# Kernel tuning notes

Measured on AMD Instinct MI355X. Metric: run time of the kernel, lower is better.

## Reference

```python
import jax, jax.numpy as jnp
import numpy as np

EPS = 1e-12
HEADS = 16
DIM_KEYS = 16
DIM_VALUES = 64


def l2norm(t):
    # matches F.normalize(t, p=2, dim=-1) with eps=1e-12
    n = jnp.linalg.norm(t, axis=-1, keepdims=True)
    return t / jnp.maximum(n, EPS)


def tanh_norm(t):
    n = jnp.linalg.norm(t, axis=-1, keepdims=True)
    return jnp.tanh(n) * (t / jnp.maximum(n, EPS))


def split_heads(x, h):
    # [b, n, h*d] -> [b, h, n, d]
    b, n, hd = x.shape
    return x.reshape(b, n, h, hd // h).transpose(0, 2, 1, 3)


def setup_inputs() -> dict:
    key = jax.random.key(0)
    k1, k2, k3, k4 = jax.random.split(key, 4)
    b, n, dim = 4, 2048, 1024
    dim_inner = (DIM_KEYS + DIM_VALUES) * HEADS  # 1280
    tokens = jax.random.normal(k1, (b, n, dim), dtype=jnp.float32)
    Wqg = jax.random.normal(k2, (dim, dim_inner), dtype=jnp.float32) * (dim ** -0.5)
    Wkv = jax.random.normal(k3, (dim, dim_inner), dtype=jnp.float32) * (dim ** -0.5)
    Wout = jax.random.normal(k4, (DIM_VALUES * HEADS, dim), dtype=jnp.float32) * ((DIM_VALUES * HEADS) ** -0.5)
    return {"tokens": tokens, "Wqg": Wqg, "Wkv": Wkv, "Wout": Wout}


def reference(tokens, Wqg, Wkv, Wout):
    # self-attention variant: context = tokens, mask = None
    qg = split_heads(tokens @ Wqg, HEADS)   # [b, h, n, dk+dv]
    kv = split_heads(tokens @ Wkv, HEADS)
    queries, gates = qg[..., :DIM_KEYS], qg[..., DIM_KEYS:]
    keys, values = kv[..., :DIM_KEYS], kv[..., DIM_KEYS:]
    queries, keys, values = l2norm(queries), l2norm(keys), l2norm(values)
    sim = jnp.einsum('bhid,bhjd->bhij', queries, keys)
    attn = jnp.square(jax.nn.relu(sim))
    aggr = jnp.einsum('bhij,bhjd->bhid', attn, values)
    out = tanh_norm(aggr) * jnp.tanh(jax.nn.silu(gates))
    b, h, n, d = out.shape
    out = out.transpose(0, 2, 1, 3).reshape(b, n, h * d)  # merge heads
    return out @ Wout
```

## Files before the change

kernel.cpp:

```cpp
#include <hip/hip_runtime.h>
#include <cstdint>
#include <cstddef>

typedef __attribute__((ext_vector_type(8))) short short8;
typedef __attribute__((ext_vector_type(8))) unsigned short ushort8;
typedef __attribute__((ext_vector_type(4))) float f32x4;
typedef __attribute__((ext_vector_type(8))) _Float16 half8;
typedef __attribute__((ext_vector_type(2))) __fp16 fp16x2;

#define DEV static __device__ __forceinline__

DEV unsigned short f2bf(float x) {
  union { float f; unsigned u; } v; v.f = x;
  unsigned r = v.u + 0x7fffu + ((v.u >> 16) & 1u);
  return (unsigned short)(r >> 16);
}
DEV float bf2f(unsigned short u) {
  union { unsigned u; float f; } v; v.u = ((unsigned)u) << 16;
  return v.f;
}
DEV unsigned pack2bf(float lo, float hi) {
  union { float f; unsigned u; } a, b; a.f = lo; b.f = hi;
  return __builtin_amdgcn_perm(b.u + 0x8000u, a.u + 0x8000u, 0x07060302u);
}
DEV f32x4 mfma16(short8 a, short8 b, f32x4 c) {
  return __builtin_amdgcn_mfma_f32_16x16x32_bf16(a, b, c, 0, 0, 0);
}
DEV f32x4 mfma16h(half8 a, half8 b, f32x4 c) {
  return __builtin_amdgcn_mfma_f32_16x16x32_f16(a, b, c, 0, 0, 0);
}

typedef __attribute__((address_space(1))) unsigned int g_u32;
typedef __attribute__((address_space(3))) unsigned int l_u32;
DEV void glds16(const unsigned short* g, unsigned short* l) {
  __builtin_amdgcn_global_load_lds((g_u32*)g, (l_u32*)l, 16, 0, 0);
}

constexpr int Bc = 4, Nc = 2048, Dc = 1024, Hc = 16, DKc = 16, DVc = 64, DIc = 1280;
constexpr int Mc = Bc * Nc;

__global__ __launch_bounds__(256) void convert_x(const float* __restrict__ X,
                                                 unsigned short* __restrict__ Xb, int total8) {
  int i = blockIdx.x * 256 + threadIdx.x;
  if (i >= total8) return;
  const float4* p = (const float4*)(X + (size_t)i * 8);
  float4 a = p[0], b = p[1];
  ushort8 o;
  o[0] = f2bf(a.x); o[1] = f2bf(a.y); o[2] = f2bf(a.z); o[3] = f2bf(a.w);
  o[4] = f2bf(b.x); o[5] = f2bf(b.y); o[6] = f2bf(b.z); o[7] = f2bf(b.w);
  *(ushort8*)(Xb + (size_t)i * 8) = o;
}

__global__ __launch_bounds__(256) void transpose_convert(const float* __restrict__ W,
                                                         unsigned short* __restrict__ WT,
                                                         int K, int N) {
  __shared__ unsigned short t[64][72];
  int k0 = blockIdx.x * 64, n0 = blockIdx.y * 64;
  int tid = threadIdx.x;
#pragma unroll
  for (int it = 0; it < 16; ++it) {
    int f = it * 256 + tid;
    int r = f >> 6, c = f & 63;
    t[c][r] = f2bf(W[(size_t)(k0 + r) * N + n0 + c]);
  }
  __syncthreads();
#pragma unroll
  for (int it = 0; it < 16; ++it) {
    int f = it * 256 + tid;
    int r = f >> 6, c = f & 63;
    WT[(size_t)(n0 + r) * K + k0 + c] = t[r][c];
  }
}

__global__ __launch_bounds__(256) void gemm_proj(const unsigned short* __restrict__ A,
                                                 const unsigned short* __restrict__ BT,
                                                 unsigned short* __restrict__ QG,
                                                 unsigned short* __restrict__ KV,
                                                 int Kq) {
  __shared__ unsigned short As[128 * 64];
  __shared__ unsigned short Bs[128 * 64];
  int row0 = blockIdx.x * 128, col0 = blockIdx.y * 128;
  int tid = threadIdx.x, lane = tid & 63, wave = tid >> 6;
  int wm = wave >> 1, wn = wave & 1;
  int ql = lane >> 4, l16 = lane & 15;
  int r8 = lane >> 3, cbl = (lane & 7) ^ r8;

  unsigned short* dst = (col0 >= DIc) ? KV : QG;
  int c0l = (col0 >= DIc) ? col0 - DIc : col0;

  const unsigned short* gA = A + (size_t)(row0 + wave * 32 + r8) * Kq + cbl * 8;
  const unsigned short* gB = BT + (size_t)(col0 + wave * 32 + r8) * Kq + cbl * 8;

  f32x4 acc[4][4];
#pragma unroll
  for (int i = 0; i < 4; i++)
#pragma unroll
    for (int j = 0; j < 4; j++) acc[i][j] = (f32x4){0.f, 0.f, 0.f, 0.f};

  for (int k0 = 0; k0 < Kq; k0 += 64) {
    __syncthreads();
#pragma unroll
    for (int i = 0; i < 4; ++i) {
      glds16(gA + (size_t)(i * 8) * Kq + k0, &As[(wave * 32 + i * 8) * 64]);
      glds16(gB + (size_t)(i * 8) * Kq + k0, &Bs[(wave * 32 + i * 8) * 64]);
    }
    __syncthreads();
#pragma unroll
    for (int kk = 0; kk < 64; kk += 32) {
      short8 af[4], bfr[4];
#pragma unroll
      for (int t = 0; t < 4; t++) {
        int row = wm * 64 + t * 16 + l16;
        int cb = (kk >> 3) + ql;
        af[t] = *(const short8*)&As[row * 64 + ((cb ^ (row & 7)) << 3)];
      }
#pragma unroll
      for (int t = 0; t < 4; t++) {
        int row = wn * 64 + t * 16 + l16;
        int cb = (kk >> 3) + ql;
        bfr[t] = *(const short8*)&Bs[row * 64 + ((cb ^ (row & 7)) << 3)];
      }
#pragma unroll
      for (int i = 0; i < 4; i++)
#pragma unroll
        for (int j = 0; j < 4; j++) acc[i][j] = mfma16(af[i], bfr[j], acc[i][j]);
    }
  }
#pragma unroll
  for (int i = 0; i < 4; i++)
#pragma unroll
    for (int j = 0; j < 4; j++)
#pragma unroll
      for (int r = 0; r < 4; r++) {
        int rr = row0 + wm * 64 + i * 16 + ql * 4 + r;
        int cc = c0l + wn * 64 + j * 16 + l16;
        dst[(size_t)rr * DIc + cc] = f2bf(acc[i][j][r]);
      }
}

__global__ __launch_bounds__(256) void gemm_glds(const unsigned short* __restrict__ A,
                                                 const unsigned short* __restrict__ BT,
                                                 float* __restrict__ Cout,
                                                 int Mq, int Nq, int Kq) {
  __shared__ unsigned short As[128 * 64];
  __shared__ unsigned short Bs[128 * 64];
  int row0 = blockIdx.x * 128, col0 = blockIdx.y * 128;
  int tid = threadIdx.x, lane = tid & 63, wave = tid >> 6;
  int wm = wave >> 1, wn = wave & 1;
  int ql = lane >> 4, l16 = lane & 15;
  int r8 = lane >> 3, cbl = (lane & 7) ^ r8;

  const unsigned short* gA = A + (size_t)(row0 + wave * 32 + r8) * Kq + cbl * 8;
  const unsigned short* gB = BT + (size_t)(col0 + wave * 32 + r8) * Kq + cbl * 8;

  f32x4 acc[4][4];
#pragma unroll
  for (int i = 0; i < 4; i++)
#pragma unroll
    for (int j = 0; j < 4; j++) acc[i][j] = (f32x4){0.f, 0.f, 0.f, 0.f};

  for (int k0 = 0; k0 < Kq; k0 += 64) {
    __syncthreads();
#pragma unroll
    for (int i = 0; i < 4; ++i) {
      glds16(gA + (size_t)(i * 8) * Kq + k0, &As[(wave * 32 + i * 8) * 64]);
      glds16(gB + (size_t)(i * 8) * Kq + k0, &Bs[(wave * 32 + i * 8) * 64]);
    }
    __syncthreads();
#pragma unroll
    for (int kk = 0; kk < 64; kk += 32) {
      short8 af[4], bfr[4];
#pragma unroll
      for (int t = 0; t < 4; t++) {
        int row = wm * 64 + t * 16 + l16;
        int cb = (kk >> 3) + ql;
        af[t] = *(const short8*)&As[row * 64 + ((cb ^ (row & 7)) << 3)];
      }
#pragma unroll
      for (int t = 0; t < 4; t++) {
        int row = wn * 64 + t * 16 + l16;
        int cb = (kk >> 3) + ql;
        bfr[t] = *(const short8*)&Bs[row * 64 + ((cb ^ (row & 7)) << 3)];
      }
#pragma unroll
      for (int i = 0; i < 4; i++)
#pragma unroll
        for (int j = 0; j < 4; j++) acc[i][j] = mfma16(af[i], bfr[j], acc[i][j]);
    }
  }
#pragma unroll
  for (int i = 0; i < 4; i++)
#pragma unroll
    for (int j = 0; j < 4; j++)
#pragma unroll
      for (int r = 0; r < 4; r++) {
        int rr = row0 + wm * 64 + i * 16 + ql * 4 + r;
        int cc = col0 + wn * 64 + j * 16 + l16;
        Cout[(size_t)rr * Nq + cc] = acc[i][j][r];
      }
}

__global__ __launch_bounds__(256) void norm_kernel(const unsigned short* __restrict__ QG,
                                                   const unsigned short* __restrict__ KV,
                                                   unsigned short* __restrict__ Qn,
                                                   unsigned short* __restrict__ Kn,
                                                   unsigned short* __restrict__ Vtg)
{
  int g = blockIdx.x * 256 + threadIdx.x;
  int n = g & (Nc - 1), bh = g >> 11;
  int h = bh & 15, b = bh >> 4;
  size_t src = ((size_t)(b * Nc + n)) * DIc + h * 80;
  const ushort8 zeros = {0, 0, 0, 0, 0, 0, 0, 0};

  {
    ushort8 u0 = *(const ushort8*)&QG[src];
    ushort8 u1 = *(const ushort8*)&QG[src + 8];
    float q[16], ss = 0.f;
#pragma unroll
    for (int i = 0; i < 8; i++) { q[i] = bf2f(u0[i]); q[8 + i] = bf2f(u1[i]); }
#pragma unroll
    for (int i = 0; i < 16; i++) ss += q[i] * q[i];
    float sc = 1.f / fmaxf(sqrtf(ss), 1e-12f);
    half8 o0, o1;
#pragma unroll
    for (int i = 0; i < 8; i++) { o0[i] = (_Float16)(q[i] * sc); o1[i] = (_Float16)(q[8 + i] * sc); }
    size_t dst = ((size_t)bh * Nc + n) * 32;
    *(half8*)&Qn[dst] = o0;
    *(half8*)&Qn[dst + 8] = o1;
    *(ushort8*)&Qn[dst + 16] = zeros;
    *(ushort8*)&Qn[dst + 24] = zeros;
  }
  {
    ushort8 u0 = *(const ushort8*)&KV[src];
    ushort8 u1 = *(const ushort8*)&KV[src + 8];
    float q[16], ss = 0.f;
#pragma unroll
    for (int i = 0; i < 8; i++) { q[i] = bf2f(u0[i]); q[8 + i] = bf2f(u1[i]); }
#pragma unroll
    for (int i = 0; i < 16; i++) ss += q[i] * q[i];
    float sc = 1.f / fmaxf(sqrtf(ss), 1e-12f);
    half8 o0, o1;
#pragma unroll
    for (int i = 0; i < 8; i++) { o0[i] = (_Float16)(q[i] * sc); o1[i] = (_Float16)(q[8 + i] * sc); }
    size_t dst = ((size_t)bh * Nc + n) * 32;
    *(half8*)&Kn[dst] = o0;
    *(half8*)&Kn[dst + 8] = o1;
    *(ushort8*)&Kn[dst + 16] = zeros;
    *(ushort8*)&Kn[dst + 24] = zeros;
  }
  {
    ushort8 u[8];
#pragma unroll
    for (int i = 0; i < 8; i++) u[i] = *(const ushort8*)&KV[src + 16 + i * 8];
    float ss = 0.f;
#pragma unroll
    for (int i = 0; i < 8; i++)
#pragma unroll
      for (int j = 0; j < 8; j++) { float x = bf2f(u[i][j]); ss += x * x; }
    float sc = 1.f / fmaxf(sqrtf(ss), 1e-12f);
#pragma unroll
    for (int i = 0; i < 8; i++)
#pragma unroll
      for (int j = 0; j < 8; j++) {
        int d = i * 8 + j;
        union { _Float16 h; unsigned short us; } cv;
        cv.h = (_Float16)(bf2f(u[i][j]) * sc);
        Vtg[((size_t)bh * DVc + d) * Nc + n] = cv.us;
      }
  }
}

__global__ __launch_bounds__(256, 4) void attn_kernel(const unsigned short* __restrict__ Qn,
                                                      const unsigned short* __restrict__ Kn,
                                                      const unsigned short* __restrict__ Vtg,
                                                      const unsigned short* __restrict__ QG,
                                                      unsigned short* __restrict__ outpre) {
  __shared__ unsigned short shm[2 * 64 * 128];

  int gid = blockIdx.x;
  int xcd = gid & 7, slot = gid >> 3;
  int bh = xcd * 8 + (slot & 7);
  int q0 = (slot >> 3) * 128;
  int b = bh >> 4, h = bh & 15;
  int tid = threadIdx.x, lane = tid & 63, wave = tid >> 6;
  int ql = lane >> 4, l16 = lane & 15;
  int qw0 = q0 + wave * 32;

  half8 qf[2];
#pragma unroll
  for (int qt = 0; qt < 2; ++qt)
    qf[qt] = *(const half8*)&Qn[((size_t)bh * Nc + qw0 + qt * 16 + l16) * 32 + ql * 8];

  const unsigned short* krow = Kn + ((size_t)bh * Nc) * 32;
  const unsigned short* vbase = Vtg + ((size_t)bh * DVc) * Nc;

  int lr = lane >> 4, m16 = lane & 15;

  f32x4 acc[4][2];
#pragma unroll
  for (int dt = 0; dt < 4; dt++) { acc[dt][0] = (f32x4){0.f,0.f,0.f,0.f}; acc[dt][1] = (f32x4){0.f,0.f,0.f,0.f}; }

#pragma unroll
  for (int i = 0; i < 4; ++i) {
    int r0 = i * 16 + wave * 4;
    int d = r0 + lr;
    glds16(vbase + (size_t)d * Nc + 0 + ((m16 ^ (d & 7)) << 3), &shm[r0 * 128]);
  }

  for (int kt = 0; kt < Nc / 128; ++kt) {
    int k0 = kt * 128;
    unsigned short* vtb = &shm[(kt & 1) * 8192];
    __syncthreads();

    half8 kf[8];
#pragma unroll
    for (int kh = 0; kh < 8; ++kh)
      kf[kh] = *(const half8*)&krow[(size_t)(k0 + kh * 16 + l16) * 32 + ql * 8];

    if (kt < Nc / 128 - 1) {
      unsigned short* nb = &shm[((kt + 1) & 1) * 8192];
      int kn0 = k0 + 128;
#pragma unroll
      for (int i = 0; i < 4; ++i) {
        int r0 = i * 16 + wave * 4;
        int d = r0 + lr;
        glds16(vbase + (size_t)d * Nc + kn0 + ((m16 ^ (d & 7)) << 3), &nb[r0 * 128]);
      }
    }

#pragma unroll
    for (int p = 0; p < 4; ++p) {
      f32x4 c0[2], c1[2];
#pragma unroll
      for (int qt = 0; qt < 2; ++qt) {
        c0[qt] = mfma16h(kf[2 * p], qf[qt], (f32x4){0.f, 0.f, 0.f, 0.f});
        c1[qt] = mfma16h(kf[2 * p + 1], qf[qt], (f32x4){0.f, 0.f, 0.f, 0.f});
      }
      half8 pf[2];
#pragma unroll
      for (int qt = 0; qt < 2; ++qt) {
        union { half8 h; fp16x2 p2[4]; } w;
        fp16x2 t0 = __builtin_amdgcn_cvt_pkrtz(c0[qt][0], c0[qt][1]);
        fp16x2 t1 = __builtin_amdgcn_cvt_pkrtz(c0[qt][2], c0[qt][3]);
        fp16x2 t2 = __builtin_amdgcn_cvt_pkrtz(c1[qt][0], c1[qt][1]);
        fp16x2 t3 = __builtin_amdgcn_cvt_pkrtz(c1[qt][2], c1[qt][3]);
        const fp16x2 hz = {(__fp16)0, (__fp16)0};
        t0 = __builtin_elementwise_max(t0, hz); w.p2[0] = t0 * t0;
        t1 = __builtin_elementwise_max(t1, hz); w.p2[1] = t1 * t1;
        t2 = __builtin_elementwise_max(t2, hz); w.p2[2] = t2 * t2;
        t3 = __builtin_elementwise_max(t3, hz); w.p2[3] = t3 * t3;
        pf[qt] = w.h;
      }
      int tsw = (l16 & 7) << 1;
      int s1 = ((p * 8 + ql) ^ tsw) << 2;
      int s2 = ((p * 8 + 4 + ql) ^ tsw) << 2;
#pragma unroll
      for (int dt = 0; dt < 4; ++dt) {
        const unsigned short* vrow = vtb + (dt * 16 + l16) * 128;
        union { half8 s; uint4 u; } vf;
        uint2 va = *(const uint2*)&vrow[s1];
        uint2 vb2 = *(const uint2*)&vrow[s2];
        vf.u.x = va.x; vf.u.y = va.y; vf.u.z = vb2.x; vf.u.w = vb2.y;
#pragma unroll
        for (int qt = 0; qt < 2; ++qt) acc[dt][qt] = mfma16h(vf.s, pf[qt], acc[dt][qt]);
      }
    }
  }

  __syncthreads();
  unsigned short(*of)[68] = (unsigned short(*)[68])shm;

#pragma unroll
  for (int qt = 0; qt < 2; ++qt) {
    float ss = 0.f;
#pragma unroll
    for (int dt = 0; dt < 4; ++dt)
#pragma unroll
      for (int r = 0; r < 4; ++r) { float v = acc[dt][qt][r]; ss += v * v; }
    ss += __shfl_xor(ss, 16, 64);
    ss += __shfl_xor(ss, 32, 64);
    float nrm = sqrtf(ss);
    float sc = tanhf(nrm) / fmaxf(nrm, 1e-12f);
    int q = qw0 + qt * 16 + l16;
    size_t gbase = ((size_t)(b * Nc + q)) * DIc + h * 80 + DKc;
#pragma unroll
    for (int dt = 0; dt < 4; ++dt) {
      uint2 gu = *(const uint2*)&QG[gbase + dt * 16 + ql * 4];
      float o[4];
#pragma unroll
      for (int r = 0; r < 4; ++r) {
        unsigned short gb = (r < 2) ? (unsigned short)(gu.x >> (16 * r))
                                    : (unsigned short)(gu.y >> (16 * (r - 2)));
        float x = bf2f(gb);
        float s = x / (1.f + __expf(-x));
        float e2 = __expf(2.f * s);
        float g = 1.f - 2.f / (e2 + 1.f);
        o[r] = acc[dt][qt][r] * sc * g;
      }
      uint2 w;
      w.x = pack2bf(o[0], o[1]);
      w.y = pack2bf(o[2], o[3]);
      *(uint2*)&of[wave * 32 + qt * 16 + l16][dt * 16 + ql * 4] = w;
    }
  }
  __syncthreads();
  {
    int row = tid >> 1, cb = (tid & 1) * 32;
    size_t obase = ((size_t)(b * Nc + q0 + row)) * (Hc * DVc) + h * DVc + cb;
#pragma unroll
    for (int i = 0; i < 4; ++i)
      *(ushort8*)&outpre[obase + i * 8] = *(const ushort8*)&of[row][cb + i * 8];
  }
}

extern "C" void kernel_launch(void* const* d_in, const int* in_sizes, int n_in,
                              void* d_out, int out_size, void* d_ws, size_t ws_size,
                              hipStream_t stream) {
  const float* X = (const float*)d_in[0];
  const float* Wqg = (const float*)d_in[1];
  const float* Wkv = (const float*)d_in[2];
  const float* Wout = (const float*)d_in[3];
  float* out = (float*)d_out;
  (void)in_sizes; (void)n_in; (void)out_size; (void)ws_size;

  char* ws = (char*)d_ws;
  size_t off = 0;
  auto alloc = [&](size_t bytes) {
    void* p = ws + off;
    off += (bytes + 255) & ~(size_t)255;
    return p;
  };
  unsigned short* Xbf   = (unsigned short*)alloc((size_t)Mc * Dc * 2);
  unsigned short* WqgT  = (unsigned short*)alloc((size_t)DIc * Dc * 2);
  unsigned short* WkvT  = (unsigned short*)alloc((size_t)DIc * Dc * 2);
  unsigned short* WoutT = (unsigned short*)alloc((size_t)Dc * Dc * 2);
  unsigned short* QG    = (unsigned short*)alloc((size_t)Mc * DIc * 2);
  unsigned short* KV    = (unsigned short*)alloc((size_t)Mc * DIc * 2);
  unsigned short* Qn    = (unsigned short*)alloc((size_t)Bc * Hc * Nc * 32 * 2);
  unsigned short* Kn    = (unsigned short*)alloc((size_t)Bc * Hc * Nc * 32 * 2);
  unsigned short* Vtg   = (unsigned short*)alloc((size_t)Bc * Hc * Nc * DVc * 2);
  unsigned short* outpre = Xbf;

  convert_x<<<(Mc * Dc / 8) / 256, 256, 0, stream>>>(X, Xbf, Mc * Dc / 8);
  transpose_convert<<<dim3(Dc / 64, DIc / 64), 256, 0, stream>>>(Wqg, WqgT, Dc, DIc);
  transpose_convert<<<dim3(Dc / 64, DIc / 64), 256, 0, stream>>>(Wkv, WkvT, Dc, DIc);
  transpose_convert<<<dim3(Dc / 64, Dc / 64), 256, 0, stream>>>(Wout, WoutT, Dc, Dc);
  gemm_proj<<<dim3(Mc / 128, 2 * DIc / 128), 256, 0, stream>>>(Xbf, WqgT, QG, KV, Dc);
  norm_kernel<<<(Mc * Hc) / 256, 256, 0, stream>>>(QG, KV, Qn, Kn, Vtg);
  attn_kernel<<<1024, 256, 0, stream>>>(Qn, Kn, Vtg, QG, outpre);
  gemm_glds<<<dim3(Mc / 128, Dc / 128), 256, 0, stream>>>(outpre, WoutT, out, Mc, Dc, Dc);
}
```

Measured before the change: 256.7 us.

## Split attention block across 8 waves with one 16-query tile per wave

The attention kernel now launches 512 threads per block, so each of 8 waves handles 16 queries instead of 32. The V tile load into shared memory is split across more waves, and K fragments are loaded per inner step instead of 8 at once. The aim is more waves to hide latency and lower register pressure per thread. In exchange each wave reloads the same K data with half the reuse, and the launch bound of 8 blocks per CU may not be reachable with the shared memory used.

```diff
diff --git a/kernel.cpp b/kernel.cpp
--- a/kernel.cpp
+++ b/kernel.cpp
@@ -270,7 +270,7 @@
   }
 }
 
-__global__ __launch_bounds__(256, 4) void attn_kernel(const unsigned short* __restrict__ Qn,
+__global__ __launch_bounds__(512, 8) void attn_kernel(const unsigned short* __restrict__ Qn,
                                                       const unsigned short* __restrict__ Kn,
                                                       const unsigned short* __restrict__ Vtg,
                                                       const unsigned short* __restrict__ QG,
@@ -284,25 +284,22 @@
   int b = bh >> 4, h = bh & 15;
   int tid = threadIdx.x, lane = tid & 63, wave = tid >> 6;
   int ql = lane >> 4, l16 = lane & 15;
-  int qw0 = q0 + wave * 32;
-
-  half8 qf[2];
-#pragma unroll
-  for (int qt = 0; qt < 2; ++qt)
-    qf[qt] = *(const half8*)&Qn[((size_t)bh * Nc + qw0 + qt * 16 + l16) * 32 + ql * 8];
+  int qw0 = q0 + wave * 16;
+
+  half8 qf = *(const half8*)&Qn[((size_t)bh * Nc + qw0 + l16) * 32 + ql * 8];
 
   const unsigned short* krow = Kn + ((size_t)bh * Nc) * 32;
   const unsigned short* vbase = Vtg + ((size_t)bh * DVc) * Nc;
 
   int lr = lane >> 4, m16 = lane & 15;
 
-  f32x4 acc[4][2];
-#pragma unroll
-  for (int dt = 0; dt < 4; dt++) { acc[dt][0] = (f32x4){0.f,0.f,0.f,0.f}; acc[dt][1] = (f32x4){0.f,0.f,0.f,0.f}; }
-
-#pragma unroll
-  for (int i = 0; i < 4; ++i) {
-    int r0 = i * 16 + wave * 4;
+  f32x4 acc[4];
+#pragma unroll
+  for (int dt = 0; dt < 4; dt++) acc[dt] = (f32x4){0.f, 0.f, 0.f, 0.f};
+
+#pragma unroll
+  for (int i = 0; i < 2; ++i) {
+    int r0 = i * 32 + wave * 4;
     int d = r0 + lr;
     glds16(vbase + (size_t)d * Nc + 0 + ((m16 ^ (d & 7)) << 3), &shm[r0 * 128]);
   }
@@ -312,17 +309,12 @@
     unsigned short* vtb = &shm[(kt & 1) * 8192];
     __syncthreads();
 
-    half8 kf[8];
-#pragma unroll
-    for (int kh = 0; kh < 8; ++kh)
-      kf[kh] = *(const half8*)&krow[(size_t)(k0 + kh * 16 + l16) * 32 + ql * 8];
-
     if (kt < Nc / 128 - 1) {
       unsigned short* nb = &shm[((kt + 1) & 1) * 8192];
       int kn0 = k0 + 128;
 #pragma unroll
-      for (int i = 0; i < 4; ++i) {
-        int r0 = i * 16 + wave * 4;
+      for (int i = 0; i < 2; ++i) {
+        int r0 = i * 32 + wave * 4;
         int d = r0 + lr;
         glds16(vbase + (size_t)d * Nc + kn0 + ((m16 ^ (d & 7)) << 3), &nb[r0 * 128]);
       }
@@ -330,26 +322,23 @@
 
 #pragma unroll
     for (int p = 0; p < 4; ++p) {
-      f32x4 c0[2], c1[2];
-#pragma unroll
-      for (int qt = 0; qt < 2; ++qt) {
-        c0[qt] = mfma16h(kf[2 * p], qf[qt], (f32x4){0.f, 0.f, 0.f, 0.f});
-        c1[qt] = mfma16h(kf[2 * p + 1], qf[qt], (f32x4){0.f, 0.f, 0.f, 0.f});
-      }
-      half8 pf[2];
-#pragma unroll
-      for (int qt = 0; qt < 2; ++qt) {
+      half8 ka = *(const half8*)&krow[(size_t)(k0 + p * 32 + l16) * 32 + ql * 8];
+      half8 kb = *(const half8*)&krow[(size_t)(k0 + p * 32 + 16 + l16) * 32 + ql * 8];
+      f32x4 c0 = mfma16h(ka, qf, (f32x4){0.f, 0.f, 0.f, 0.f});
+      f32x4 c1 = mfma16h(kb, qf, (f32x4){0.f, 0.f, 0.f, 0.f});
+      half8 pf;
+      {
         union { half8 h; fp16x2 p2[4]; } w;
-        fp16x2 t0 = __builtin_amdgcn_cvt_pkrtz(c0[qt][0], c0[qt][1]);
-        fp16x2 t1 = __builtin_amdgcn_cvt_pkrtz(c0[qt][2], c0[qt][3]);
-        fp16x2 t2 = __builtin_amdgcn_cvt_pkrtz(c1[qt][0], c1[qt][1]);
-        fp16x2 t3 = __builtin_amdgcn_cvt_pkrtz(c1[qt][2], c1[qt][3]);
+        fp16x2 t0 = __builtin_amdgcn_cvt_pkrtz(c0[0], c0[1]);
+        fp16x2 t1 = __builtin_amdgcn_cvt_pkrtz(c0[2], c0[3]);
+        fp16x2 t2 = __builtin_amdgcn_cvt_pkrtz(c1[0], c1[1]);
+        fp16x2 t3 = __builtin_amdgcn_cvt_pkrtz(c1[2], c1[3]);
         const fp16x2 hz = {(__fp16)0, (__fp16)0};
         t0 = __builtin_elementwise_max(t0, hz); w.p2[0] = t0 * t0;
         t1 = __builtin_elementwise_max(t1, hz); w.p2[1] = t1 * t1;
         t2 = __builtin_elementwise_max(t2, hz); w.p2[2] = t2 * t2;
         t3 = __builtin_elementwise_max(t3, hz); w.p2[3] = t3 * t3;
-        pf[qt] = w.h;
+        pf = w.h;
       }
       int tsw = (l16 & 7) << 1;
       int s1 = ((p * 8 + ql) ^ tsw) << 2;
@@ -361,8 +350,7 @@
         uint2 va = *(const uint2*)&vrow[s1];
         uint2 vb2 = *(const uint2*)&vrow[s2];
         vf.u.x = va.x; vf.u.y = va.y; vf.u.z = vb2.x; vf.u.w = vb2.y;
-#pragma unroll
-        for (int qt = 0; qt < 2; ++qt) acc[dt][qt] = mfma16h(vf.s, pf[qt], acc[dt][qt]);
+        acc[dt] = mfma16h(vf.s, pf, acc[dt]);
       }
     }
   }
@@ -370,18 +358,17 @@
   __syncthreads();
   unsigned short(*of)[68] = (unsigned short(*)[68])shm;
 
-#pragma unroll
-  for (int qt = 0; qt < 2; ++qt) {
+  {
     float ss = 0.f;
 #pragma unroll
     for (int dt = 0; dt < 4; ++dt)
 #pragma unroll
-      for (int r = 0; r < 4; ++r) { float v = acc[dt][qt][r]; ss += v * v; }
+      for (int r = 0; r < 4; ++r) { float v = acc[dt][r]; ss += v * v; }
     ss += __shfl_xor(ss, 16, 64);
     ss += __shfl_xor(ss, 32, 64);
     float nrm = sqrtf(ss);
     float sc = tanhf(nrm) / fmaxf(nrm, 1e-12f);
-    int q = qw0 + qt * 16 + l16;
+    int q = qw0 + l16;
     size_t gbase = ((size_t)(b * Nc + q)) * DIc + h * 80 + DKc;
 #pragma unroll
     for (int dt = 0; dt < 4; ++dt) {
@@ -395,21 +382,20 @@
         float s = x / (1.f + __expf(-x));
         float e2 = __expf(2.f * s);
         float g = 1.f - 2.f / (e2 + 1.f);
-        o[r] = acc[dt][qt][r] * sc * g;
+        o[r] = acc[dt][r] * sc * g;
       }
       uint2 w;
       w.x = pack2bf(o[0], o[1]);
       w.y = pack2bf(o[2], o[3]);
-      *(uint2*)&of[wave * 32 + qt * 16 + l16][dt * 16 + ql * 4] = w;
+      *(uint2*)&of[wave * 16 + l16][dt * 16 + ql * 4] = w;
     }
   }
   __syncthreads();
   {
-    int row = tid >> 1, cb = (tid & 1) * 32;
-    size_t obase = ((size_t)(b * Nc + q0 + row)) * (Hc * DVc) + h * DVc + cb;
-#pragma unroll
-    for (int i = 0; i < 4; ++i)
-      *(ushort8*)&outpre[obase + i * 8] = *(const ushort8*)&of[row][cb + i * 8];
+    int row = tid >> 2, seg = tid & 3;
+    size_t obase = ((size_t)(b * Nc + q0 + row)) * (Hc * DVc) + h * DVc + seg * 16;
+    *(ushort8*)&outpre[obase] = *(const ushort8*)&of[row][seg * 16];
+    *(ushort8*)&outpre[obase + 8] = *(const ushort8*)&of[row][seg * 16 + 8];
   }
 }
 
@@ -447,6 +433,6 @@
   transpose_convert<<<dim3(Dc / 64, Dc / 64), 256, 0, stream>>>(Wout, WoutT, Dc, Dc);
   gemm_proj<<<dim3(Mc / 128, 2 * DIc / 128), 256, 0, stream>>>(Xbf, WqgT, QG, KV, Dc);
   norm_kernel<<<(Mc * Hc) / 256, 256, 0, stream>>>(QG, KV, Qn, Kn, Vtg);
-  attn_kernel<<<1024, 256, 0, stream>>>(Qn, Kn, Vtg, QG, outpre);
+  attn_kernel<<<1024, 512, 0, stream>>>(Qn, Kn, Vtg, QG, outpre);
   gemm_glds<<<dim3(Mc / 128, Dc / 128), 256, 0, stream>>>(outpre, WoutT, out, Mc, Dc, Dc);
 }
```

Result: slower. 277.2 us (+8.0%).
